# Kernel tuning notes

Hardware: AMD Instinct MI355X
Metric: run time of the kernel (lower is better)

Reference implementation:

```python
import jax, jax.numpy as jnp
import numpy as np

TEMPERATURE = 0.5


def setup_inputs() -> dict:
    key = jax.random.key(0)
    k1, k2 = jax.random.split(key)
    N, Z = 4096, 2048
    z1 = jax.random.normal(k1, (N, Z), dtype=jnp.float32)
    z2 = jax.random.normal(k2, (N, Z), dtype=jnp.float32)
    return {"z1": z1, "z2": z2}


def reference(z1, z2):
    # NT-Xent loss. Original torch code: normalize, build full 2Nx2N cosine-sim
    # matrix, prepend the positive pair column, cross-entropy with label 0.
    # Mathematically, per-row CE with the positive prepended and the self-sim
    # removed equals: logsumexp over the row excluding the diagonal, minus the
    # positive logit.  (cosine_similarity on already-normalized vectors is a
    # plain dot product, so normalization is applied once.)
    n, _ = z1.shape
    a = z1 / jnp.linalg.norm(z1, axis=1, keepdims=True)  # [N, Z]
    b = z2 / jnp.linalg.norm(z2, axis=1, keepdims=True)  # [N, Z]
    reps = jnp.concatenate([a, b], axis=0)               # [2N, Z]
    logits = jnp.matmul(reps, reps.T) / TEMPERATURE      # [2N, 2N]
    NEG_INF = jnp.float32(-1e9)  # mask self-similarity (excluded from CE denom)
    logits = jnp.where(jnp.eye(2 * n, dtype=bool), NEG_INF, logits)
    pos = jnp.sum(a * b, axis=1) / TEMPERATURE           # [N] positive logits
    pos = jnp.concatenate([pos, pos])                    # [2N]
    lse = jax.nn.logsumexp(logits, axis=1)               # [2N]
    # sum of CE over 2N rows, divided by 2N  == mean
    return jnp.mean(lse - pos)
```

## Files before the change

kernel.cpp:

```cpp
#include <hip/hip_runtime.h>
#include <stdint.h>

#define N_ROWS 4096
#define Z_DIM  2048
#define TOT    8192
#define TILE   128
#define BKB    128
#define NITER  (Z_DIM / BKB)
#define NT     (TOT / TILE)
#define NBLK   (NT * (NT + 1) / 2)
#define INV_T  2.0f
#define SCL    16.0f

typedef __attribute__((ext_vector_type(4))) int   intx4;
typedef __attribute__((ext_vector_type(8))) int   intx8;
typedef __attribute__((ext_vector_type(4))) float floatx4;

#define GLOAD16(g, l)                                                   \
    __builtin_amdgcn_global_load_lds(                                   \
        (const __attribute__((address_space(1))) unsigned int*)(g),     \
        (__attribute__((address_space(3))) unsigned int*)(l), 16, 0, 0)

__global__ __launch_bounds__(256) void normalize_kernel(
    const float* __restrict__ z1, const float* __restrict__ z2,
    unsigned char* __restrict__ reps, float* __restrict__ pos,
    float* __restrict__ rowsum)
{
    const int row  = blockIdx.x;
    const int tid  = threadIdx.x;
    const int lane = tid & 63, wave = tid >> 6;

    if (row < TOT / 256) rowsum[row * 256 + tid] = 0.f;

    const float4* p1 = (const float4*)(z1 + (size_t)row * Z_DIM);
    const float4* p2 = (const float4*)(z2 + (size_t)row * Z_DIM);
    float4 x0 = p1[tid * 2], x1 = p1[tid * 2 + 1];
    float4 y0 = p2[tid * 2], y1 = p2[tid * 2 + 1];

    float s1 = x0.x*x0.x + x0.y*x0.y + x0.z*x0.z + x0.w*x0.w
             + x1.x*x1.x + x1.y*x1.y + x1.z*x1.z + x1.w*x1.w;
    float s2 = y0.x*y0.x + y0.y*y0.y + y0.z*y0.z + y0.w*y0.w
             + y1.x*y1.x + y1.y*y1.y + y1.z*y1.z + y1.w*y1.w;
    float dd = x0.x*y0.x + x0.y*y0.y + x0.z*y0.z + x0.w*y0.w
             + x1.x*y1.x + x1.y*y1.y + x1.z*y1.z + x1.w*y1.w;

    #pragma unroll
    for (int m = 1; m < 64; m <<= 1) {
        s1 += __shfl_xor(s1, m);
        s2 += __shfl_xor(s2, m);
        dd += __shfl_xor(dd, m);
    }
    __shared__ float red[3][4];
    if (lane == 0) { red[0][wave] = s1; red[1][wave] = s2; red[2][wave] = dd; }
    __syncthreads();
    s1 = red[0][0] + red[0][1] + red[0][2] + red[0][3];
    s2 = red[1][0] + red[1][1] + red[1][2] + red[1][3];
    dd = red[2][0] + red[2][1] + red[2][2] + red[2][3];

    const float inv1 = rsqrtf(s1), inv2 = rsqrtf(s2);
    if (tid == 0) {
        float p = dd * inv1 * inv2 * INV_T;
        pos[row] = p;
        pos[row + N_ROWS] = p;
    }

    const float a = inv1 * SCL, b = inv2 * SCL;
    unsigned int a0 = 0, a1 = 0, b0 = 0, b1 = 0;
    a0 = __builtin_amdgcn_cvt_pk_fp8_f32(x0.x * a, x0.y * a, a0, false);
    a0 = __builtin_amdgcn_cvt_pk_fp8_f32(x0.z * a, x0.w * a, a0, true);
    a1 = __builtin_amdgcn_cvt_pk_fp8_f32(x1.x * a, x1.y * a, a1, false);
    a1 = __builtin_amdgcn_cvt_pk_fp8_f32(x1.z * a, x1.w * a, a1, true);
    b0 = __builtin_amdgcn_cvt_pk_fp8_f32(y0.x * b, y0.y * b, b0, false);
    b0 = __builtin_amdgcn_cvt_pk_fp8_f32(y0.z * b, y0.w * b, b0, true);
    b1 = __builtin_amdgcn_cvt_pk_fp8_f32(y1.x * b, y1.y * b, b1, false);
    b1 = __builtin_amdgcn_cvt_pk_fp8_f32(y1.z * b, y1.w * b, b1, true);
    uint2 pa = {a0, a1}, pb = {b0, b1};
    *(uint2*)(reps + (size_t)row * Z_DIM + tid * 8) = pa;
    *(uint2*)(reps + (size_t)(N_ROWS + row) * Z_DIM + tid * 8) = pb;
}

__global__ __launch_bounds__(256) void simclr_gemm(
    const unsigned char* __restrict__ reps, float* __restrict__ rowsum)
{
    __shared__ __align__(16) unsigned char L[2][2][TILE * BKB];

    const int t = blockIdx.x;
    int r = (int)((sqrtf(8.0f * (float)t + 1.0f) - 1.0f) * 0.5f);
    while ((r + 1) * (r + 2) / 2 <= t) ++r;
    while (r * (r + 1) / 2 > t) --r;
    const int bi = t - r * (r + 1) / 2;
    const int bj = r;
    const bool diag = (bi == bj);

    const int tid  = threadIdx.x;
    const int lane = tid & 63, wave = tid >> 6;
    const int wr = wave >> 1, wc = wave & 1;
    const int quad = lane >> 4, l16 = lane & 15;
    const int sw   = l16 & 7;
    const int row0 = bi * TILE, col0 = bj * TILE;

    floatx4 acc[4][4];
    #pragma unroll
    for (int i = 0; i < 4; ++i)
        #pragma unroll
        for (int j = 0; j < 4; ++j)
            acc[i][j] = floatx4{0.f, 0.f, 0.f, 0.f};

    const unsigned char* gA[4]; const unsigned char* gB[4];
    int ldsOff[4];
    #pragma unroll
    for (int q = 0; q < 4; ++q) {
        const int c = q * 256 + tid;
        const int srow = c >> 3, gkc = (c & 7) ^ (srow & 7);
        gA[q] = reps + (size_t)(row0 + srow) * Z_DIM + gkc * 16;
        gB[q] = reps + (size_t)(col0 + srow) * Z_DIM + gkc * 16;
        ldsOff[q] = c * 16;
    }

    #pragma unroll
    for (int q = 0; q < 4; ++q) GLOAD16(gA[q], &L[0][0][ldsOff[q]]);
    #pragma unroll
    for (int q = 0; q < 4; ++q) GLOAD16(gB[q], &L[0][1][ldsOff[q]]);
    __syncthreads();

    for (int i = 0; i < NITER; ++i) {
        if (i + 1 < NITER) {
            const size_t ko = (size_t)(i + 1) * BKB;
            const int buf = (i + 1) & 1;
            #pragma unroll
            for (int q = 0; q < 4; ++q) GLOAD16(gA[q] + ko, &L[buf][0][ldsOff[q]]);
            #pragma unroll
            for (int q = 0; q < 4; ++q) GLOAD16(gB[q] + ko, &L[buf][1][ldsOff[q]]);
        }
        const unsigned char* Ab = &L[i & 1][0][0];
        const unsigned char* Bb = &L[i & 1][1][0];

        intx8 af[4], bf[4];
        #pragma unroll
        for (int fi = 0; fi < 4; ++fi) {
            const int ar = (wr * 64 + fi * 16 + l16) * BKB;
            const int br = (wc * 64 + fi * 16 + l16) * BKB;
            intx4 alo = *(const intx4*)&Ab[ar + (((quad * 2)     ^ sw) << 4)];
            intx4 ahi = *(const intx4*)&Ab[ar + (((quad * 2 + 1) ^ sw) << 4)];
            intx4 blo = *(const intx4*)&Bb[br + (((quad * 2)     ^ sw) << 4)];
            intx4 bhi = *(const intx4*)&Bb[br + (((quad * 2 + 1) ^ sw) << 4)];
            af[fi] = intx8{alo[0], alo[1], alo[2], alo[3], ahi[0], ahi[1], ahi[2], ahi[3]};
            bf[fi] = intx8{blo[0], blo[1], blo[2], blo[3], bhi[0], bhi[1], bhi[2], bhi[3]};
        }
        #pragma unroll
        for (int fi = 0; fi < 4; ++fi)
            #pragma unroll
            for (int j = 0; j < 4; ++j)
                acc[fi][j] = __builtin_amdgcn_mfma_scale_f32_16x16x128_f8f6f4(
                    af[fi], bf[j], acc[fi][j],
                    0, 0,
                    0, 0x7F7F7F7Fu,
                    0, 0x7F7F7F7Fu);
        __syncthreads();
    }

    const float descale = INV_T / (SCL * SCL);
    float scol[4] = {0.f, 0.f, 0.f, 0.f};
    #pragma unroll
    for (int fi = 0; fi < 4; ++fi) {
        const int rbase = row0 + wr * 64 + fi * 16 + quad * 4;
        float srow[4] = {0.f, 0.f, 0.f, 0.f};
        #pragma unroll
        for (int j = 0; j < 4; ++j) {
            const int c = col0 + wc * 64 + j * 16 + l16;
            #pragma unroll
            for (int rr = 0; rr < 4; ++rr) {
                float e = __expf(acc[fi][j][rr] * descale);
                if (diag && (rbase + rr == c)) e = 0.f;
                srow[rr] += e;
                scol[j]  += e;
            }
        }
        #pragma unroll
        for (int rr = 0; rr < 4; ++rr) {
            #pragma unroll
            for (int m = 1; m < 16; m <<= 1) srow[rr] += __shfl_xor(srow[rr], m);
        }
        if (l16 == 0) {
            #pragma unroll
            for (int rr = 0; rr < 4; ++rr)
                atomicAdd(&rowsum[rbase + rr], srow[rr]);
        }
    }
    if (!diag) {
        #pragma unroll
        for (int j = 0; j < 4; ++j) {
            scol[j] += __shfl_xor(scol[j], 16);
            scol[j] += __shfl_xor(scol[j], 32);
        }
        if (quad == 0) {
            #pragma unroll
            for (int j = 0; j < 4; ++j)
                atomicAdd(&rowsum[col0 + wc * 64 + j * 16 + l16], scol[j]);
        }
    }
}

__global__ __launch_bounds__(1024) void finalize_kernel(
    const float* __restrict__ rowsum, const float* __restrict__ pos,
    float* __restrict__ out)
{
    const int tid = threadIdx.x;
    const int lane = tid & 63, wave = tid >> 6;
    float s = 0.f;
    for (int r = tid; r < TOT; r += 1024) s += logf(rowsum[r]) - pos[r];
    #pragma unroll
    for (int m = 1; m < 64; m <<= 1) s += __shfl_xor(s, m);
    __shared__ float red[16];
    if (lane == 0) red[wave] = s;
    __syncthreads();
    if (tid == 0) {
        float t = 0.f;
        #pragma unroll
        for (int w = 0; w < 16; ++w) t += red[w];
        out[0] = t * (1.0f / TOT);
    }
}

extern "C" void kernel_launch(void* const* d_in, const int* in_sizes, int n_in,
                              void* d_out, int out_size, void* d_ws, size_t ws_size,
                              hipStream_t stream)
{
    const float* z1 = (const float*)d_in[0];
    const float* z2 = (const float*)d_in[1];
    float* out = (float*)d_out;

    char* w = (char*)d_ws;
    unsigned char* reps = (unsigned char*)w;
    float* pos    = (float*)(w + (size_t)TOT * Z_DIM);
    float* rowsum = pos + TOT;

    normalize_kernel<<<N_ROWS, 256, 0, stream>>>(z1, z2, reps, pos, rowsum);
    simclr_gemm<<<NBLK, 256, 0, stream>>>(reps, rowsum);
    finalize_kernel<<<1, 1024, 0, stream>>>(rowsum, pos, out);
}
```

Measured before the change: 181.8 us.

## Quantize normalized embeddings to FP4 and run the Gram GEMM with FP4 MFMA

Replaces the FP8 quantization of the normalized representations with a manual FP4 (e2m1) encoder, packing two values per byte and using scale 64 instead of 16. The GEMM loads half as many bytes per K step and runs the scaled MFMA in FP4 mode (format code 4), with LDS tiles, swizzle and descale adjusted to match. This halves the memory traffic and raises matrix throughput. The cost is much coarser precision in the similarity logits, which may push the loss outside tolerance.

```diff
diff --git a/kernel.cpp b/kernel.cpp
--- a/kernel.cpp
+++ b/kernel.cpp
@@ -5,12 +5,14 @@
 #define Z_DIM  2048
 #define TOT    8192
 #define TILE   128
-#define BKB    128
-#define NITER  (Z_DIM / BKB)
+#define RBYTES (Z_DIM / 2)
+#define BKE    128
+#define KBYT   (BKE / 2)
+#define NITER  (Z_DIM / BKE)
 #define NT     (TOT / TILE)
 #define NBLK   (NT * (NT + 1) / 2)
 #define INV_T  2.0f
-#define SCL    16.0f
+#define SCL4   64.0f
 
 typedef __attribute__((ext_vector_type(4))) int   intx4;
 typedef __attribute__((ext_vector_type(8))) int   intx8;
@@ -20,6 +22,13 @@
     __builtin_amdgcn_global_load_lds(                                   \
         (const __attribute__((address_space(1))) unsigned int*)(g),     \
         (__attribute__((address_space(3))) unsigned int*)(l), 16, 0, 0)
+
+__device__ __forceinline__ unsigned int f2fp4(float v) {
+    float a = fabsf(v);
+    unsigned int c = (a >= 0.25f) + (a >= 0.75f) + (a >= 1.25f) + (a >= 1.75f)
+                   + (a >= 2.5f)  + (a >= 3.5f)  + (a >= 5.0f);
+    return c | (v < 0.f ? 8u : 0u);
+}
 
 __global__ __launch_bounds__(256) void normalize_kernel(
     const float* __restrict__ z1, const float* __restrict__ z2,
@@ -64,25 +73,23 @@
         pos[row + N_ROWS] = p;
     }
 
-    const float a = inv1 * SCL, b = inv2 * SCL;
-    unsigned int a0 = 0, a1 = 0, b0 = 0, b1 = 0;
-    a0 = __builtin_amdgcn_cvt_pk_fp8_f32(x0.x * a, x0.y * a, a0, false);
-    a0 = __builtin_amdgcn_cvt_pk_fp8_f32(x0.z * a, x0.w * a, a0, true);
-    a1 = __builtin_amdgcn_cvt_pk_fp8_f32(x1.x * a, x1.y * a, a1, false);
-    a1 = __builtin_amdgcn_cvt_pk_fp8_f32(x1.z * a, x1.w * a, a1, true);
-    b0 = __builtin_amdgcn_cvt_pk_fp8_f32(y0.x * b, y0.y * b, b0, false);
-    b0 = __builtin_amdgcn_cvt_pk_fp8_f32(y0.z * b, y0.w * b, b0, true);
-    b1 = __builtin_amdgcn_cvt_pk_fp8_f32(y1.x * b, y1.y * b, b1, false);
-    b1 = __builtin_amdgcn_cvt_pk_fp8_f32(y1.z * b, y1.w * b, b1, true);
-    uint2 pa = {a0, a1}, pb = {b0, b1};
-    *(uint2*)(reps + (size_t)row * Z_DIM + tid * 8) = pa;
-    *(uint2*)(reps + (size_t)(N_ROWS + row) * Z_DIM + tid * 8) = pb;
+    const float a = inv1 * SCL4, b = inv2 * SCL4;
+    unsigned int pa =  f2fp4(x0.x * a)        | (f2fp4(x0.y * a) << 4)
+                    | (f2fp4(x0.z * a) << 8)  | (f2fp4(x0.w * a) << 12)
+                    | (f2fp4(x1.x * a) << 16) | (f2fp4(x1.y * a) << 20)
+                    | (f2fp4(x1.z * a) << 24) | (f2fp4(x1.w * a) << 28);
+    unsigned int pb =  f2fp4(y0.x * b)        | (f2fp4(y0.y * b) << 4)
+                    | (f2fp4(y0.z * b) << 8)  | (f2fp4(y0.w * b) << 12)
+                    | (f2fp4(y1.x * b) << 16) | (f2fp4(y1.y * b) << 20)
+                    | (f2fp4(y1.z * b) << 24) | (f2fp4(y1.w * b) << 28);
+    *(unsigned int*)(reps + (size_t)row * RBYTES + tid * 4) = pa;
+    *(unsigned int*)(reps + (size_t)(N_ROWS + row) * RBYTES + tid * 4) = pb;
 }
 
 __global__ __launch_bounds__(256) void simclr_gemm(
     const unsigned char* __restrict__ reps, float* __restrict__ rowsum)
 {
-    __shared__ __align__(16) unsigned char L[2][2][TILE * BKB];
+    __shared__ __align__(16) unsigned char L[2][2][TILE * KBYT];
 
     const int t = blockIdx.x;
     int r = (int)((sqrtf(8.0f * (float)t + 1.0f) - 1.0f) * 0.5f);
@@ -96,7 +103,7 @@
     const int lane = tid & 63, wave = tid >> 6;
     const int wr = wave >> 1, wc = wave & 1;
     const int quad = lane >> 4, l16 = lane & 15;
-    const int sw   = l16 & 7;
+    const int sw   = l16 & 3;
     const int row0 = bi * TILE, col0 = bj * TILE;
 
     floatx4 acc[4][4];
@@ -106,31 +113,29 @@
         for (int j = 0; j < 4; ++j)
             acc[i][j] = floatx4{0.f, 0.f, 0.f, 0.f};
 
-    const unsigned char* gA[4]; const unsigned char* gB[4];
-    int ldsOff[4];
-    #pragma unroll
-    for (int q = 0; q < 4; ++q) {
-        const int c = q * 256 + tid;
-        const int srow = c >> 3, gkc = (c & 7) ^ (srow & 7);
-        gA[q] = reps + (size_t)(row0 + srow) * Z_DIM + gkc * 16;
-        gB[q] = reps + (size_t)(col0 + srow) * Z_DIM + gkc * 16;
-        ldsOff[q] = c * 16;
-    }
-
-    #pragma unroll
-    for (int q = 0; q < 4; ++q) GLOAD16(gA[q], &L[0][0][ldsOff[q]]);
-    #pragma unroll
-    for (int q = 0; q < 4; ++q) GLOAD16(gB[q], &L[0][1][ldsOff[q]]);
+    const int c0 = tid, c1 = tid + 256;
+    const int r0s = c0 >> 2, k0s = (c0 & 3) ^ (r0s & 3);
+    const int r1s = c1 >> 2, k1s = (c1 & 3) ^ (r1s & 3);
+    const unsigned char* gA0 = reps + (size_t)(row0 + r0s) * RBYTES + k0s * 16;
+    const unsigned char* gA1 = reps + (size_t)(row0 + r1s) * RBYTES + k1s * 16;
+    const unsigned char* gB0 = reps + (size_t)(col0 + r0s) * RBYTES + k0s * 16;
+    const unsigned char* gB1 = reps + (size_t)(col0 + r1s) * RBYTES + k1s * 16;
+    const int o0 = c0 * 16, o1 = c1 * 16;
+
+    GLOAD16(gA0, &L[0][0][o0]);
+    GLOAD16(gA1, &L[0][0][o1]);
+    GLOAD16(gB0, &L[0][1][o0]);
+    GLOAD16(gB1, &L[0][1][o1]);
     __syncthreads();
 
     for (int i = 0; i < NITER; ++i) {
         if (i + 1 < NITER) {
-            const size_t ko = (size_t)(i + 1) * BKB;
+            const size_t ko = (size_t)(i + 1) * KBYT;
             const int buf = (i + 1) & 1;
-            #pragma unroll
-            for (int q = 0; q < 4; ++q) GLOAD16(gA[q] + ko, &L[buf][0][ldsOff[q]]);
-            #pragma unroll
-            for (int q = 0; q < 4; ++q) GLOAD16(gB[q] + ko, &L[buf][1][ldsOff[q]]);
+            GLOAD16(gA0 + ko, &L[buf][0][o0]);
+            GLOAD16(gA1 + ko, &L[buf][0][o1]);
+            GLOAD16(gB0 + ko, &L[buf][1][o0]);
+            GLOAD16(gB1 + ko, &L[buf][1][o1]);
         }
         const unsigned char* Ab = &L[i & 1][0][0];
         const unsigned char* Bb = &L[i & 1][1][0];
@@ -138,14 +143,12 @@
         intx8 af[4], bf[4];
         #pragma unroll
         for (int fi = 0; fi < 4; ++fi) {
-            const int ar = (wr * 64 + fi * 16 + l16) * BKB;
-            const int br = (wc * 64 + fi * 16 + l16) * BKB;
-            intx4 alo = *(const intx4*)&Ab[ar + (((quad * 2)     ^ sw) << 4)];
-            intx4 ahi = *(const intx4*)&Ab[ar + (((quad * 2 + 1) ^ sw) << 4)];
-            intx4 blo = *(const intx4*)&Bb[br + (((quad * 2)     ^ sw) << 4)];
-            intx4 bhi = *(const intx4*)&Bb[br + (((quad * 2 + 1) ^ sw) << 4)];
-            af[fi] = intx8{alo[0], alo[1], alo[2], alo[3], ahi[0], ahi[1], ahi[2], ahi[3]};
-            bf[fi] = intx8{blo[0], blo[1], blo[2], blo[3], bhi[0], bhi[1], bhi[2], bhi[3]};
+            const int ar = (wr * 64 + fi * 16 + l16) * KBYT;
+            const int br = (wc * 64 + fi * 16 + l16) * KBYT;
+            intx4 av = *(const intx4*)&Ab[ar + ((quad ^ sw) << 4)];
+            intx4 bv = *(const intx4*)&Bb[br + ((quad ^ sw) << 4)];
+            af[fi] = intx8{av[0], av[1], av[2], av[3], 0, 0, 0, 0};
+            bf[fi] = intx8{bv[0], bv[1], bv[2], bv[3], 0, 0, 0, 0};
         }
         #pragma unroll
         for (int fi = 0; fi < 4; ++fi)
@@ -153,13 +156,13 @@
             for (int j = 0; j < 4; ++j)
                 acc[fi][j] = __builtin_amdgcn_mfma_scale_f32_16x16x128_f8f6f4(
                     af[fi], bf[j], acc[fi][j],
-                    0, 0,
+                    4, 4,
                     0, 0x7F7F7F7Fu,
                     0, 0x7F7F7F7Fu);
         __syncthreads();
     }
 
-    const float descale = INV_T / (SCL * SCL);
+    const float descale = INV_T / (SCL4 * SCL4);
     float scol[4] = {0.f, 0.f, 0.f, 0.f};
     #pragma unroll
     for (int fi = 0; fi < 4; ++fi) {
@@ -232,7 +235,7 @@
 
     char* w = (char*)d_ws;
     unsigned char* reps = (unsigned char*)w;
-    float* pos    = (float*)(w + (size_t)TOT * Z_DIM);
+    float* pos    = (float*)(w + (size_t)TOT * RBYTES);
     float* rowsum = pos + TOT;
 
     normalize_kernel<<<N_ROWS, 256, 0, stream>>>(z1, z2, reps, pos, rowsum);
```

Result: faster. 155.7 us (-14.4%).
